# Kernel optimization log

Hardware: AMD Instinct MI355X
Metric: run time of the kernel (lower is better)

Reference implementation:

```python
import jax, jax.numpy as jnp
import numpy as np

NUM_EXPERTS = 8
PHM_DIM = 4


def setup_inputs() -> dict:
    key = jax.random.key(0)
    k1, k2, k3, k4 = jax.random.split(key, 4)
    bsz, seq, D, O, E, p = 4, 2048, 2048, 2048, NUM_EXPERTS, PHM_DIM
    hidden_states = jax.random.normal(k1, (bsz, seq, D), dtype=jnp.float32)
    gate_w = jax.random.normal(k2, (D, E), dtype=jnp.float32) * 0.02
    phm_rule = jax.random.normal(k3, (E, p, p, p), dtype=jnp.float32) * 0.1
    W = jax.random.normal(k4, (E, p, D // p, O // p), dtype=jnp.float32) * 0.02
    b = jnp.zeros((E, O), dtype=jnp.float32)
    return {"hidden_states": hidden_states, "gate_w": gate_w,
            "phm_rule": phm_rule, "W": W, "b": b}


def reference(hidden_states, gate_w, phm_rule, W, b):
    bsz, seq, dim = hidden_states.shape
    E = gate_w.shape[1]
    x = hidden_states.reshape(-1, dim)                      # [T, D]
    logits = x @ gate_w                                     # [T, E]
    prob = jax.nn.softmax(logits, axis=-1)                  # [T, E]
    gate = jnp.argmax(prob, axis=-1)                        # [T]
    # load-balancing loss
    num_tokens = jnp.sum(jax.nn.one_hot(gate, E, dtype=jnp.int32), axis=0)  # [E]
    f = num_tokens.astype(prob.dtype)
    f = f / jnp.sum(f)
    P = jnp.mean(prob, axis=0)
    balance_loss = E * jnp.sum(P * f)
    # PHM weight per expert: H_e = sum_p kron(phm_rule[e,p], W[e,p]) -> [E, D, O]
    Wfull = jnp.einsum('epab,epij->eaibj', phm_rule, W).reshape(E, dim, -1)
    # dense evaluation of every expert on every token, then top-1 select
    all_out = jnp.einsum('td,edo->teo', x, Wfull) + b[None, :, :]  # [T, E, O]
    tok_prob = jnp.take_along_axis(prob, gate[:, None], axis=1)    # [T, 1]
    out = jnp.take_along_axis(all_out, gate[:, None, None], axis=1)[:, 0, :] * tok_prob
    out = out.reshape(bsz, seq, -1)
    return out, balance_loss, num_tokens
```

## Files before the change

kernel.cpp:

```cpp
#include <hip/hip_runtime.h>
#include <cstdint>
#include <cstddef>

typedef _Float16 f16;
typedef f16 f16x2 __attribute__((ext_vector_type(2)));
typedef f16 f16x4 __attribute__((ext_vector_type(4)));
typedef f16 f16x8 __attribute__((ext_vector_type(8)));
typedef float f32x4 __attribute__((ext_vector_type(4)));

#define NEXP 8
#define BM 256
#define BN 256
#define BK 64

__device__ __forceinline__ void async_cp16(void* lds, const void* gsrc) {
  __builtin_amdgcn_global_load_lds(
      (const __attribute__((address_space(1))) void*)gsrc,
      (__attribute__((address_space(3))) void*)lds, 16, 0, 0);
}

__global__ __launch_bounds__(256) void k_gwT(const float* __restrict__ gw,
                                             float* __restrict__ gwT, int D) {
  int i = blockIdx.x * 256 + threadIdx.x;
  int e = i / D, d = i - e * D;
  gwT[i] = gw[d * NEXP + e];
}

__global__ __launch_bounds__(256) void k_gate(
    const float* __restrict__ x, const float* __restrict__ gwT,
    f16* __restrict__ xb, int* __restrict__ gate, float* __restrict__ scale,
    int* __restrict__ cnt, float* __restrict__ probsum, int D)
{
  __shared__ float ps[NEXP];
  __shared__ int pc[NEXP];
  int tid = threadIdx.x, lane = tid & 63, w = tid >> 6;
  if (tid < NEXP) { ps[tid] = 0.f; pc[tid] = 0; }
  __syncthreads();

  int t = blockIdx.x * 4 + w;
  const float* xr = x + (size_t)t * D;
  f16* xbr = xb + (size_t)t * D;

  float acc[NEXP] = {};
  for (int d0 = lane * 4; d0 < D; d0 += 256) {
    float4 v = *(const float4*)(xr + d0);
    f16x4 h; h[0] = (f16)v.x; h[1] = (f16)v.y; h[2] = (f16)v.z; h[3] = (f16)v.w;
    *(f16x4*)(xbr + d0) = h;
#pragma unroll
    for (int e = 0; e < NEXP; e++) {
      float4 g = *(const float4*)(gwT + (size_t)e * D + d0);
      acc[e] += v.x * g.x + v.y * g.y + v.z * g.z + v.w * g.w;
    }
  }
#pragma unroll
  for (int e = 0; e < NEXP; e++) {
    float v = acc[e];
    for (int o = 32; o > 0; o >>= 1) v += __shfl_xor(v, o);
    acc[e] = v;
  }
  if (lane == 0) {
    float m = acc[0]; int g = 0;
#pragma unroll
    for (int e = 1; e < NEXP; e++) if (acc[e] > m) { m = acc[e]; g = e; }
    float pr[NEXP]; float ssum = 0.f;
#pragma unroll
    for (int e = 0; e < NEXP; e++) { pr[e] = __expf(acc[e] - m); ssum += pr[e]; }
    float inv = 1.0f / ssum;
#pragma unroll
    for (int e = 0; e < NEXP; e++) atomicAdd(&ps[e], pr[e] * inv);
    atomicAdd(&pc[g], 1);
    gate[t] = g;
    scale[t] = pr[g] * inv;
  }
  __syncthreads();
  if (tid < NEXP) {
    atomicAdd(&probsum[tid], ps[tid]);
    atomicAdd(&cnt[tid], pc[tid]);
  }
}

__global__ __launch_bounds__(256) void k_wfull(
    const float* __restrict__ Wp, const float* __restrict__ rule,
    f16* __restrict__ wt, int Dp, int Op, int D, int O)
{
  int bid = blockIdx.x;
  int it = Dp >> 5, jt = Op >> 5;
  int itile = bid % it; bid /= it;
  int jtile = bid % jt; bid /= jt;
  int e = bid;
  int i0 = itile * 32, j0 = jtile * 32;

  __shared__ float Wt[4][32][33];
  int tid = threadIdx.x;
  for (int idx = tid; idx < 4096; idx += 256) {
    int p = idx >> 10, rem = idx & 1023, ii = rem >> 5, jj = rem & 31;
    Wt[p][ii][jj] = Wp[(size_t)((e * 4 + p) * Dp + i0 + ii) * Op + j0 + jj];
  }
  __syncthreads();

  int ii = (tid & 15) * 2, jjb = tid >> 4;
#pragma unroll
  for (int b = 0; b < 4; b++) {
    float s[4][4];
#pragma unroll
    for (int p = 0; p < 4; p++)
#pragma unroll
      for (int a = 0; a < 4; a++)
        s[p][a] = rule[((e * 4 + p) * 4 + a) * 4 + b];
#pragma unroll
    for (int a = 0; a < 4; a++) {
#pragma unroll
      for (int jp = 0; jp < 2; jp++) {
        int jj = jjb + jp * 16;
        float v0 = 0.f, v1 = 0.f;
#pragma unroll
        for (int p = 0; p < 4; p++) {
          v0 += s[p][a] * Wt[p][ii][jj];
          v1 += s[p][a] * Wt[p][ii + 1][jj];
        }
        size_t n = (size_t)b * Op + j0 + jj;
        size_t dd = (size_t)a * Dp + i0 + ii;
        f16x2 hv; hv[0] = (f16)v0; hv[1] = (f16)v1;
        *(f16x2*)(wt + ((size_t)e * O + n) * D + dd) = hv;
      }
    }
  }
}

__global__ __launch_bounds__(128) void k_plan(
    const int* __restrict__ cnt, const float* __restrict__ probsum,
    int* __restrict__ offs, int* __restrict__ ndesc,
    int2* __restrict__ desc, float* __restrict__ otail, int T)
{
  __shared__ int soffs[NEXP + 1];
  __shared__ int snd;
  __shared__ float sloss;
  __shared__ int2 sdesc[96];
  int tid = threadIdx.x;
  if (tid == 0) {
    int off = 0, nd = 0; float loss = 0.f;
    for (int e = 0; e < NEXP; e++) {
      soffs[e] = off;
      int c = cnt[e];
      loss += probsum[e] * (float)c;
      for (int m0 = 0; m0 < c; m0 += BM) { sdesc[nd] = make_int2(e, m0); nd++; }
      off += c;
    }
    soffs[NEXP] = off;
    snd = nd;
    sloss = loss;
  }
  __syncthreads();
  if (tid <= NEXP) offs[tid] = soffs[tid];
  if (tid == 9) *ndesc = snd;
  if (tid == 10) {
    float invT = 1.0f / (float)T;
    otail[0] = (float)NEXP * sloss * invT * invT;
  }
  if (tid >= 16 && tid < 16 + NEXP) otail[1 + tid - 16] = (float)cnt[tid - 16];
  for (int i = tid; i < snd; i += 128) desc[i] = sdesc[i];
}

__global__ __launch_bounds__(256) void k_scatter(
    const int* __restrict__ gate, const int* __restrict__ offs,
    int* __restrict__ cursor, int* __restrict__ perm)
{
  int t = blockIdx.x * 256 + threadIdx.x;
  int g = gate[t];
  int lane = threadIdx.x & 63;
  int pos = 0;
#pragma unroll
  for (int e = 0; e < NEXP; e++) {
    unsigned long long mask = __ballot(g == e);
    if (mask == 0ull) continue;
    int leader = __ffsll((unsigned long long)mask) - 1;
    int base = 0;
    if (lane == leader) base = atomicAdd(&cursor[e], (int)__popcll(mask));
    base = __shfl(base, leader);
    if (g == e) {
      int below = (int)__popcll(mask & ((1ull << lane) - 1ull));
      pos = offs[e] + base + below;
    }
  }
  perm[pos] = t;
}

__global__ __launch_bounds__(512) void k_gemm(
    const f16* __restrict__ xb, const f16* __restrict__ wt,
    const float* __restrict__ bias, const int* __restrict__ perm,
    const int* __restrict__ cnt, const int* __restrict__ offs,
    const int* __restrict__ ndesc, const int2* __restrict__ desc,
    const float* __restrict__ scale, float* __restrict__ out, int D, int O)
{
  if ((int)blockIdx.y >= *ndesc) return;
  int2 dsc = desc[blockIdx.y];
  int e = dsc.x, m0 = dsc.y;
  int ce = cnt[e];
  int seg = offs[e];
  int n0 = blockIdx.x * BN;

  __shared__ f16 As[2][BM * BK];
  __shared__ f16 Bs[2][BN * BK];
  __shared__ int tokS[BM];
  __shared__ float scS[BM];

  int tid = threadIdx.x;
  if (tid < BM) {
    int idx = m0 + tid; if (idx > ce - 1) idx = ce - 1;
    int tok = perm[seg + idx];
    tokS[tid] = tok;
    scS[tid] = scale[tok];
  }
  __syncthreads();

  int sr = tid >> 3, sc = tid & 7;
  uint32_t offA[4], offB[4];
#pragma unroll
  for (int rr = 0; rr < 4; rr++) {
    int row = sr + rr * 64;
    int gc = sc ^ (row & 7);
    offA[rr] = ((uint32_t)tokS[row] * (uint32_t)D + (uint32_t)(gc * 8)) * 2u;
    offB[rr] = ((uint32_t)(e * O + n0 + row) * (uint32_t)D + (uint32_t)(gc * 8)) * 2u;
  }

#define STAGE(kk, pb)                                                         \
  do {                                                                        \
    _Pragma("unroll")                                                         \
    for (int rr = 0; rr < 4; rr++)                                            \
      async_cp16(&As[pb][rr * 4096 + tid * 8],                                \
                 (const char*)xb + offA[rr] + (kk) * (BK * 2));               \
    _Pragma("unroll")                                                         \
    for (int rr = 0; rr < 4; rr++)                                            \
      async_cp16(&Bs[pb][rr * 4096 + tid * 8],                                \
                 (const char*)wt + offB[rr] + (kk) * (BK * 2));               \
  } while (0)

  int lane = tid & 63;
  int wid = tid >> 6;
  int wr = wid >> 2, wc = wid & 3;
  int lr = lane & 15, q = lane >> 4;
  int aoff = (wr * 128 + lr) * BK;
  int boff = (wc * 64 + lr) * BK;
  int s0 = ((q ^ (lr & 7)) * 8);
  int s1 = s0 ^ 32;

  f32x4 acc[8][4] = {};
  int nkt = D / BK;

  STAGE(0, 0);
  STAGE(1, 1);
  asm volatile("s_waitcnt vmcnt(8)\n\ts_barrier" ::: "memory");

#pragma unroll 2
  for (int kt = 0; kt < nkt; ++kt) {
    int p = kt & 1;
    const f16* Ab = As[p];
    const f16* Bb = Bs[p];
    f16x8 a0[4], a1[4], a2[4], a3[4], b0[4], b1[4];

#pragma unroll
    for (int i = 0; i < 4; i++) {
      a0[i] = *(const f16x8*)&Ab[aoff + (i * 16) * BK + s0];
      b0[i] = *(const f16x8*)&Bb[boff + (i * 16) * BK + s0];
    }
#pragma unroll
    for (int i = 0; i < 4; i++)
      a1[i] = *(const f16x8*)&Ab[aoff + ((i + 4) * 16) * BK + s0];

    __builtin_amdgcn_s_setprio(1);
#pragma unroll
    for (int mi = 0; mi < 4; mi++)
#pragma unroll
      for (int ni = 0; ni < 4; ni++)
        acc[mi][ni] = __builtin_amdgcn_mfma_f32_16x16x32_f16(
            a0[mi], b0[ni], acc[mi][ni], 0, 0, 0);
    __builtin_amdgcn_s_setprio(0);

#pragma unroll
    for (int i = 0; i < 4; i++) {
      a2[i] = *(const f16x8*)&Ab[aoff + (i * 16) * BK + s1];
      b1[i] = *(const f16x8*)&Bb[boff + (i * 16) * BK + s1];
    }

    __builtin_amdgcn_s_setprio(1);
#pragma unroll
    for (int mi = 0; mi < 4; mi++)
#pragma unroll
      for (int ni = 0; ni < 4; ni++)
        acc[mi + 4][ni] = __builtin_amdgcn_mfma_f32_16x16x32_f16(
            a1[mi], b0[ni], acc[mi + 4][ni], 0, 0, 0);
    __builtin_amdgcn_s_setprio(0);

#pragma unroll
    for (int i = 0; i < 4; i++)
      a3[i] = *(const f16x8*)&Ab[aoff + ((i + 4) * 16) * BK + s1];

    __builtin_amdgcn_s_setprio(1);
#pragma unroll
    for (int mi = 0; mi < 4; mi++)
#pragma unroll
      for (int ni = 0; ni < 4; ni++)
        acc[mi][ni] = __builtin_amdgcn_mfma_f32_16x16x32_f16(
            a2[mi], b1[ni], acc[mi][ni], 0, 0, 0);
    __builtin_amdgcn_s_setprio(0);

    asm volatile("s_waitcnt lgkmcnt(0)\n\ts_barrier" ::: "memory");
    if (kt + 2 < nkt) STAGE(kt + 2, p);

    __builtin_amdgcn_s_setprio(1);
#pragma unroll
    for (int mi = 0; mi < 4; mi++)
#pragma unroll
      for (int ni = 0; ni < 4; ni++)
        acc[mi + 4][ni] = __builtin_amdgcn_mfma_f32_16x16x32_f16(
            a3[mi], b1[ni], acc[mi + 4][ni], 0, 0, 0);
    __builtin_amdgcn_s_setprio(0);

    if (kt + 2 < nkt)
      asm volatile("s_waitcnt vmcnt(8)\n\ts_barrier" ::: "memory");
    else if (kt + 1 < nkt)
      asm volatile("s_waitcnt vmcnt(0)\n\ts_barrier" ::: "memory");
  }
#undef STAGE

  float bv[4];
#pragma unroll
  for (int ni = 0; ni < 4; ni++)
    bv[ni] = bias[(size_t)e * O + n0 + wc * 64 + ni * 16 + lr];
#pragma unroll
  for (int mi = 0; mi < 8; mi++) {
#pragma unroll
    for (int rg = 0; rg < 4; rg++) {
      int rl = wr * 128 + mi * 16 + q * 4 + rg;
      if (m0 + rl < ce) {
        float s = scS[rl];
        float* orow = out + (size_t)tokS[rl] * O + n0 + wc * 64;
#pragma unroll
        for (int ni = 0; ni < 4; ni++)
          orow[ni * 16 + lr] = (acc[mi][ni][rg] + bv[ni]) * s;
      }
    }
  }
}

extern "C" void kernel_launch(void* const* d_in, const int* in_sizes, int n_in,
                              void* d_out, int out_size, void* d_ws, size_t ws_size,
                              hipStream_t stream)
{
  const float* x    = (const float*)d_in[0];
  const float* gw   = (const float*)d_in[1];
  const float* rule = (const float*)d_in[2];
  const float* W    = (const float*)d_in[3];
  const float* bias = (const float*)d_in[4];
  float* out = (float*)d_out;

  int D = in_sizes[1] / NEXP;
  int O = in_sizes[4] / NEXP;
  int T = in_sizes[0] / D;
  int Dp = D / 4, Op = O / 4;

  uint8_t* ws = (uint8_t*)d_ws;
  size_t off = 0;
  f16* xb = (f16*)(ws + off);  off += (size_t)T * D * 2;
  f16* wt = (f16*)(ws + off);  off += (size_t)NEXP * O * D * 2;
  int*   gate  = (int*)(ws + off);   off += (size_t)T * 4;
  float* scale = (float*)(ws + off); off += (size_t)T * 4;
  int*   perm  = (int*)(ws + off);   off += (size_t)T * 4;
  off = (off + 255) & ~(size_t)255;
  uint8_t* C = ws + off;
  int*   cnt     = (int*)(C + 0);
  float* probsum = (float*)(C + 32);
  int*   cursor  = (int*)(C + 64);
  int*   ndesc   = (int*)(C + 96);
  int*   offs    = (int*)(C + 128);
  int2*  desc    = (int2*)(C + 192);
  float* gwT     = (float*)(C + 4096);

  hipMemsetAsync(C, 0, 128, stream);

  k_gwT<<<(NEXP * D) / 256, 256, 0, stream>>>(gw, gwT, D);
  k_gate<<<T / 4, 256, 0, stream>>>(x, gwT, xb, gate, scale, cnt, probsum, D);
  k_wfull<<<NEXP * (Op / 32) * (Dp / 32), 256, 0, stream>>>(W, rule, wt, Dp, Op, D, O);
  k_plan<<<1, 128, 0, stream>>>(cnt, probsum, offs, ndesc, desc, out + (size_t)T * O, T);
  k_scatter<<<T / 256, 256, 0, stream>>>(gate, offs, cursor, perm);

  int maxdesc = T / BM + NEXP;
  k_gemm<<<dim3(O / BN, maxdesc), 512, 0, stream>>>(
      xb, wt, bias, perm, cnt, offs, ndesc, desc, scale, out, D, O);
}
```

Before: 354.3 us.

## Restructure grouped GEMM main loop into four-phase interleaved load/MFMA schedule

Splits each K-tile into four phases that interleave LDS fragment reads, partial async global-to-LDS staging of A and B, and 16-MFMA clusters, with barriers between phases. This spreads memory traffic across the iteration instead of issuing all loads at once. It also swaps the grid axes so consecutive blocks walk token tiles for a fixed N slice, and sets launch_bounds(512,2) to request two blocks per CU. The added barriers and the register pressure from the occupancy target may introduce stalls or spills.

```diff
diff --git a/kernel.cpp b/kernel.cpp
--- a/kernel.cpp
+++ b/kernel.cpp
@@ -185,19 +185,19 @@
   perm[pos] = t;
 }
 
-__global__ __launch_bounds__(512) void k_gemm(
+__global__ __launch_bounds__(512, 2) void k_gemm(
     const f16* __restrict__ xb, const f16* __restrict__ wt,
     const float* __restrict__ bias, const int* __restrict__ perm,
     const int* __restrict__ cnt, const int* __restrict__ offs,
     const int* __restrict__ ndesc, const int2* __restrict__ desc,
     const float* __restrict__ scale, float* __restrict__ out, int D, int O)
 {
-  if ((int)blockIdx.y >= *ndesc) return;
-  int2 dsc = desc[blockIdx.y];
+  if ((int)blockIdx.x >= *ndesc) return;
+  int2 dsc = desc[blockIdx.x];
   int e = dsc.x, m0 = dsc.y;
   int ce = cnt[e];
   int seg = offs[e];
-  int n0 = blockIdx.x * BN;
+  int n0 = blockIdx.y * BN;
 
   __shared__ f16 As[2][BM * BK];
   __shared__ f16 Bs[2][BN * BK];
@@ -223,121 +223,132 @@
     offB[rr] = ((uint32_t)(e * O + n0 + row) * (uint32_t)D + (uint32_t)(gc * 8)) * 2u;
   }
 
-#define STAGE(kk, pb)                                                         \
+#define STAGE_A(kk, pb, r0)                                                   \
   do {                                                                        \
     _Pragma("unroll")                                                         \
-    for (int rr = 0; rr < 4; rr++)                                            \
+    for (int rr = (r0); rr < (r0) + 2; rr++)                                  \
       async_cp16(&As[pb][rr * 4096 + tid * 8],                                \
-                 (const char*)xb + offA[rr] + (kk) * (BK * 2));               \
+                 (const char*)xb + offA[rr] + (uint32_t)(kk) * (BK * 2));     \
+  } while (0)
+#define STAGE_B(kk, pb, r0)                                                   \
+  do {                                                                        \
     _Pragma("unroll")                                                         \
-    for (int rr = 0; rr < 4; rr++)                                            \
+    for (int rr = (r0); rr < (r0) + 2; rr++)                                  \
       async_cp16(&Bs[pb][rr * 4096 + tid * 8],                                \
-                 (const char*)wt + offB[rr] + (kk) * (BK * 2));               \
+                 (const char*)wt + offB[rr] + (uint32_t)(kk) * (BK * 2));     \
   } while (0)
 
   int lane = tid & 63;
   int wid = tid >> 6;
   int wr = wid >> 2, wc = wid & 3;
   int lr = lane & 15, q = lane >> 4;
-  int aoff = (wr * 128 + lr) * BK;
-  int boff = (wc * 64 + lr) * BK;
-  int s0 = ((q ^ (lr & 7)) * 8);
-  int s1 = s0 ^ 32;
-
-  f32x4 acc[8][4] = {};
+  int abase = wr * 8192 + lr * 64;
+  int bbase = wc * 4096 + lr * 64;
+  const int slotk[2] = { ((0 * 4 + q) ^ (lr & 7)) * 8,
+                         ((1 * 4 + q) ^ (lr & 7)) * 8 };
+
+#define READ_A(mh, ks)                                                        \
+  _Pragma("unroll")                                                           \
+  for (int mi = 0; mi < 4; mi++)                                              \
+    af[mi] = *(const f16x8*)&Ab[abase + (mh) * 4096 + mi * 1024 + slotk[ks]];
+#define READ_B(ks)                                                            \
+  _Pragma("unroll")                                                           \
+  for (int nh = 0; nh < 2; nh++)                                              \
+    _Pragma("unroll")                                                         \
+    for (int ni = 0; ni < 2; ni++)                                            \
+      bf[ks][nh][ni] =                                                        \
+          *(const f16x8*)&Bb[bbase + nh * 2048 + ni * 1024 + slotk[ks]];
+#define MFMA16(mh, ks)                                                        \
+  do {                                                                        \
+    __builtin_amdgcn_s_setprio(1);                                            \
+    _Pragma("unroll")                                                         \
+    for (int mi = 0; mi < 4; mi++)                                            \
+      _Pragma("unroll")                                                       \
+      for (int nh = 0; nh < 2; nh++)                                          \
+        _Pragma("unroll")                                                     \
+        for (int ni = 0; ni < 2; ni++)                                        \
+          acc[mh][mi][nh][ni] = __builtin_amdgcn_mfma_f32_16x16x32_f16(       \
+              af[mi], bf[ks][nh][ni], acc[mh][mi][nh][ni], 0, 0, 0);          \
+    __builtin_amdgcn_s_setprio(0);                                            \
+  } while (0)
+#define PBAR __builtin_amdgcn_s_barrier()
+#define LGKM0 asm volatile("s_waitcnt lgkmcnt(0)" ::: "memory")
+
+  f32x4 acc[2][4][2][2] = {};
   int nkt = D / BK;
 
-  STAGE(0, 0);
-  STAGE(1, 1);
+  STAGE_A(0, 0, 0); STAGE_A(0, 0, 2);
+  STAGE_B(0, 0, 0); STAGE_B(0, 0, 2);
+  STAGE_A(1, 1, 0); STAGE_A(1, 1, 2);
+  STAGE_B(1, 1, 0); STAGE_B(1, 1, 2);
   asm volatile("s_waitcnt vmcnt(8)\n\ts_barrier" ::: "memory");
 
-#pragma unroll 2
+#pragma unroll 1
   for (int kt = 0; kt < nkt; ++kt) {
-    int p = kt & 1;
-    const f16* Ab = As[p];
-    const f16* Bb = Bs[p];
-    f16x8 a0[4], a1[4], a2[4], a3[4], b0[4], b1[4];
-
-#pragma unroll
-    for (int i = 0; i < 4; i++) {
-      a0[i] = *(const f16x8*)&Ab[aoff + (i * 16) * BK + s0];
-      b0[i] = *(const f16x8*)&Bb[boff + (i * 16) * BK + s0];
-    }
-#pragma unroll
-    for (int i = 0; i < 4; i++)
-      a1[i] = *(const f16x8*)&Ab[aoff + ((i + 4) * 16) * BK + s0];
-
-    __builtin_amdgcn_s_setprio(1);
-#pragma unroll
-    for (int mi = 0; mi < 4; mi++)
-#pragma unroll
-      for (int ni = 0; ni < 4; ni++)
-        acc[mi][ni] = __builtin_amdgcn_mfma_f32_16x16x32_f16(
-            a0[mi], b0[ni], acc[mi][ni], 0, 0, 0);
-    __builtin_amdgcn_s_setprio(0);
-
-#pragma unroll
-    for (int i = 0; i < 4; i++) {
-      a2[i] = *(const f16x8*)&Ab[aoff + (i * 16) * BK + s1];
-      b1[i] = *(const f16x8*)&Bb[boff + (i * 16) * BK + s1];
-    }
-
-    __builtin_amdgcn_s_setprio(1);
-#pragma unroll
-    for (int mi = 0; mi < 4; mi++)
-#pragma unroll
-      for (int ni = 0; ni < 4; ni++)
-        acc[mi + 4][ni] = __builtin_amdgcn_mfma_f32_16x16x32_f16(
-            a1[mi], b0[ni], acc[mi + 4][ni], 0, 0, 0);
-    __builtin_amdgcn_s_setprio(0);
-
-#pragma unroll
-    for (int i = 0; i < 4; i++)
-      a3[i] = *(const f16x8*)&Ab[aoff + ((i + 4) * 16) * BK + s1];
-
-    __builtin_amdgcn_s_setprio(1);
-#pragma unroll
-    for (int mi = 0; mi < 4; mi++)
-#pragma unroll
-      for (int ni = 0; ni < 4; ni++)
-        acc[mi][ni] = __builtin_amdgcn_mfma_f32_16x16x32_f16(
-            a2[mi], b1[ni], acc[mi][ni], 0, 0, 0);
-    __builtin_amdgcn_s_setprio(0);
-
-    asm volatile("s_waitcnt lgkmcnt(0)\n\ts_barrier" ::: "memory");
-    if (kt + 2 < nkt) STAGE(kt + 2, p);
-
-    __builtin_amdgcn_s_setprio(1);
-#pragma unroll
-    for (int mi = 0; mi < 4; mi++)
-#pragma unroll
-      for (int ni = 0; ni < 4; ni++)
-        acc[mi + 4][ni] = __builtin_amdgcn_mfma_f32_16x16x32_f16(
-            a3[mi], b1[ni], acc[mi + 4][ni], 0, 0, 0);
-    __builtin_amdgcn_s_setprio(0);
-
-    if (kt + 2 < nkt)
-      asm volatile("s_waitcnt vmcnt(8)\n\ts_barrier" ::: "memory");
-    else if (kt + 1 < nkt)
-      asm volatile("s_waitcnt vmcnt(0)\n\ts_barrier" ::: "memory");
-  }
-#undef STAGE
-
-  float bv[4];
-#pragma unroll
-  for (int ni = 0; ni < 4; ni++)
-    bv[ni] = bias[(size_t)e * O + n0 + wc * 64 + ni * 16 + lr];
-#pragma unroll
-  for (int mi = 0; mi < 8; mi++) {
-#pragma unroll
-    for (int rg = 0; rg < 4; rg++) {
-      int rl = wr * 128 + mi * 16 + q * 4 + rg;
-      if (m0 + rl < ce) {
-        float s = scS[rl];
-        float* orow = out + (size_t)tokS[rl] * O + n0 + wc * 64;
-#pragma unroll
-        for (int ni = 0; ni < 4; ni++)
-          orow[ni * 16 + lr] = (acc[mi][ni][rg] + bv[ni]) * s;
+    int pb = kt & 1;
+    const f16* Ab = &As[pb][0];
+    const f16* Bb = &Bs[pb][0];
+    f16x8 af[4], bf[2][2][2];
+    bool stA = (kt >= 1) && (kt + 1 < nkt);
+    bool stB = (kt + 2 < nkt);
+
+    READ_A(0, 0); READ_B(0);
+    if (stA) STAGE_A(kt + 1, pb ^ 1, 0);
+    PBAR; LGKM0;
+    MFMA16(0, 0);
+    PBAR;
+
+    READ_A(0, 1); READ_B(1);
+    if (stA) STAGE_A(kt + 1, pb ^ 1, 2);
+    PBAR; LGKM0;
+    MFMA16(0, 1);
+    PBAR;
+
+    READ_A(1, 0);
+    if (stB) STAGE_B(kt + 2, pb, 0);
+    PBAR; LGKM0;
+    MFMA16(1, 0);
+    PBAR;
+
+    READ_A(1, 1);
+    if (stB) STAGE_B(kt + 2, pb, 2);
+    PBAR; LGKM0;
+    MFMA16(1, 1);
+    if (stB) asm volatile("s_waitcnt vmcnt(4)" ::: "memory");
+    else     asm volatile("s_waitcnt vmcnt(0)" ::: "memory");
+    PBAR;
+  }
+#undef STAGE_A
+#undef STAGE_B
+#undef READ_A
+#undef READ_B
+#undef MFMA16
+#undef PBAR
+#undef LGKM0
+
+  float bv[2][2];
+#pragma unroll
+  for (int nh = 0; nh < 2; nh++)
+#pragma unroll
+    for (int ni = 0; ni < 2; ni++)
+      bv[nh][ni] = bias[(size_t)e * O + n0 + wc * 64 + nh * 32 + ni * 16 + lr];
+#pragma unroll
+  for (int mh = 0; mh < 2; mh++) {
+#pragma unroll
+    for (int mi = 0; mi < 4; mi++) {
+#pragma unroll
+      for (int rg = 0; rg < 4; rg++) {
+        int rl = wr * 128 + mh * 64 + mi * 16 + q * 4 + rg;
+        if (m0 + rl < ce) {
+          float s = scS[rl];
+          float* orow = out + (size_t)tokS[rl] * O + n0 + wc * 64;
+#pragma unroll
+          for (int nh = 0; nh < 2; nh++)
+#pragma unroll
+            for (int ni = 0; ni < 2; ni++)
+              orow[nh * 32 + ni * 16 + lr] =
+                  (acc[mh][mi][nh][ni][rg] + bv[nh][ni]) * s;
+        }
       }
     }
   }
@@ -385,6 +396,6 @@
   k_scatter<<<T / 256, 256, 0, stream>>>(gate, offs, cursor, perm);
 
   int maxdesc = T / BM + NEXP;
-  k_gemm<<<dim3(O / BN, maxdesc), 512, 0, stream>>>(
+  k_gemm<<<dim3(maxdesc, O / BN), 512, 0, stream>>>(
       xb, wt, bias, perm, cnt, offs, ndesc, desc, scale, out, D, O);
 }
```

Measured after the change: 364.2 us. 2.8% more time.
